# Kernel optimization log

Hardware: AMD Instinct MI355X
Metric: run time of the kernel (lower is better)

## Reference

```python
import jax, jax.numpy as jnp
import numpy as np
import math

HIDDEN = 2048
HEADS = 16
HEAD_DIM = HIDDEN // HEADS
MAX_SEQ = 4096
ROPE_BASE = 10000.0


def rope_cos_sin(seq_len):
    # (seq_len, head_dim//2) angle table
    inv_freq = 1.0 / (ROPE_BASE ** (jnp.arange(0, HEAD_DIM, 2, dtype=jnp.float32) / HEAD_DIM))
    t = jnp.arange(seq_len, dtype=jnp.float32)
    ang = jnp.einsum('s,f->sf', t, inv_freq)
    return jnp.cos(ang), jnp.sin(ang)


def apply_rope(x, cos, sin):
    # x: (b, s, h, d); interleaved complex pairs along last dim
    b, s, h, d = x.shape
    xr = x.reshape(b, s, h, d // 2, 2)
    x0, x1 = xr[..., 0], xr[..., 1]
    c = cos[:s][None, :, None, :]
    sn = sin[:s][None, :, None, :]
    o0 = x0 * c - x1 * sn
    o1 = x0 * sn + x1 * c
    return jnp.stack([o0, o1], axis=-1).reshape(b, s, h, d)


def setup_inputs() -> dict:
    key = jax.random.key(0)
    k1, k2, k3, k4, k5, k6 = jax.random.split(key, 6)
    B, SQ, SK = 2, 2048, 2048
    x = jax.random.normal(k1, (B, SQ, HIDDEN), dtype=jnp.float32)
    enc = jax.random.normal(k2, (B, SK, HIDDEN), dtype=jnp.float32)
    mask = jnp.ones((B, SK), dtype=jnp.int32)
    scale = 0.02
    Wq = jax.random.normal(k3, (HIDDEN, HIDDEN), dtype=jnp.float32) * scale
    Wk = jax.random.normal(k4, (HIDDEN, HIDDEN), dtype=jnp.float32) * scale
    Wv = jax.random.normal(k5, (HIDDEN, HIDDEN), dtype=jnp.float32) * scale
    Wo = jax.random.normal(k6, (HIDDEN, HIDDEN), dtype=jnp.float32) * scale
    return {"x": x, "encoder_output": enc, "encoder_attention_mask": mask,
            "Wq": Wq, "Wk": Wk, "Wv": Wv, "Wo": Wo}


def reference(x, encoder_output, encoder_attention_mask, Wq, Wk, Wv, Wo):
    B, SQ, _ = x.shape
    SK = encoder_output.shape[1]
    # nn.Linear(bias=False): y = x @ W^T
    q = (x @ Wq.T).reshape(B, SQ, HEADS, HEAD_DIM)
    k = (encoder_output @ Wk.T).reshape(B, SK, HEADS, HEAD_DIM)
    v = (encoder_output @ Wv.T).reshape(B, SK, HEADS, HEAD_DIM)
    cos, sin = rope_cos_sin(max(SQ, SK))
    q = apply_rope(q, cos, sin)
    k = apply_rope(k, cos, sin)
    scale = math.sqrt(HEAD_DIM)
    # (b, h, sq, sk) scores
    scores = jnp.einsum('bqhd,bkhd->bhqk', q, k) / scale
    mask = encoder_attention_mask[:, None, None, :]
    scores = jnp.where(mask == 0, -jnp.inf, scores)
    attn = jax.nn.softmax(scores, axis=-1)
    out = jnp.einsum('bhqk,bkhd->bqhd', attn, v).reshape(B, SQ, HIDDEN)
    return out @ Wo.T
```

## Files before the change

kernel.cpp:

```cpp
#include <hip/hip_runtime.h>
#include <stdint.h>


#define LOG2E 1.44269504088896340736f
#define INV2PI 0.15915494309189535f

typedef __attribute__((ext_vector_type(8))) short bf16x8;
typedef __attribute__((ext_vector_type(8))) uint16_t u16x8;
typedef __attribute__((ext_vector_type(4))) uint16_t u16x4;
typedef __attribute__((ext_vector_type(4))) float f32x4;

__device__ __forceinline__ uint16_t f2bf(float f) {
  union { float f; uint32_t i; } v; v.f = f;
  uint32_t x = v.i;
  return (uint16_t)((x + 0x7fffu + ((x >> 16) & 1u)) >> 16);
}
__device__ __forceinline__ uint32_t f_as_u(float f) { union { float f; uint32_t u; } v; v.f = f; return v.u; }
__device__ __forceinline__ float u_as_f(uint32_t u) { union { uint32_t u; float f; } v; v.u = u; return v.f; }
__device__ __forceinline__ void glds16(const void* g, void* l) {
  __builtin_amdgcn_global_load_lds((const __attribute__((address_space(1))) void*)g,
                                   (__attribute__((address_space(3))) void*)l, 16, 0, 0);
}

__global__ __launch_bounds__(256) void convert_f32_bf16(const float* __restrict__ in,
                                                        uint16_t* __restrict__ out) {
  const long i = ((long)blockIdx.x * 256 + threadIdx.x) * 8;
  const f32x4 a = *(const f32x4*)(in + i);
  const f32x4 b = *(const f32x4*)(in + i + 4);
  u16x8 o;
#pragma unroll
  for (int j = 0; j < 4; ++j) { o[j] = f2bf(a[j]); o[4 + j] = f2bf(b[j]); }
  *(u16x8*)(out + i) = o;
}

__global__ __launch_bounds__(256) void mask_bias(const int* __restrict__ m,
                                                 float* __restrict__ bias) {
  const int i = blockIdx.x * 256 + threadIdx.x;
  bias[i] = m[i] ? 0.0f : -__builtin_inff();
}

#define EPI_ROPE 0
#define EPI_KV   1
#define EPI_F32  2

__device__ __forceinline__ void epi_rope_store(uint16_t* C, const f32x4& a, int rowbase,
                                               int col, int N, float oscale) {
  const int f = (col >> 1) & 63;
  const float inv = __builtin_amdgcn_exp2f((float)f * (-13.287712379549449f / 64.0f));
  const float sgn = (col & 1) ? 1.0f : -1.0f;
#pragma unroll
  for (int r = 0; r < 4; ++r) {
    const float val = a[r];
    const float partner = __shfl_xor(val, 1);
    const int s = (rowbase + r) & 2047;
    const float rev = __builtin_amdgcn_fractf((float)s * inv * INV2PI);
    const float sn = __builtin_amdgcn_sinf(rev);
    const float cs = __builtin_amdgcn_cosf(rev);
    C[(long)(rowbase + r) * N + col] = f2bf((val * cs + sgn * partner * sn) * oscale);
  }
}

template <int MODE>
__global__ __launch_bounds__(256) void gemm_bt(const uint16_t* __restrict__ A,
                                               const uint16_t* __restrict__ W0,
                                               const uint16_t* __restrict__ W1,
                                               void* __restrict__ C0v,
                                               void* __restrict__ C1v,
                                               int M, int N, int K, float oscale) {
  __shared__ __align__(16) uint16_t As[2][128 * 32];
  __shared__ __align__(16) uint16_t Bs[2][128 * 32];
  const int tid = threadIdx.x;
  const int lane = tid & 63;
  const int w = tid >> 6;
  const int r16 = lane & 15, quad = lane >> 4;
  const int m0 = blockIdx.y * 128, n0 = blockIdx.x * 128;
  const int wm = (w >> 1) * 64, wn = (w & 1) * 64;
  f32x4 acc[4][4] = {};
  const int srow = 32 * w + (lane >> 2);
  const int scol = (lane & 3) * 8;
  const uint16_t* Wbase = (MODE == EPI_KV && n0 >= 2048) ? W1 + (long)(n0 - 2048) * K
                                                         : W0 + (long)n0 * K;
  const uint16_t* Ag = A + (long)(m0 + srow) * K + scol;
  const uint16_t* Wg = Wbase + (long)srow * K + scol;
  const int co = 2 * w * 512;

  glds16(Ag, &As[0][co]);
  glds16(Ag + (long)16 * K, &As[0][co + 512]);
  glds16(Wg, &Bs[0][co]);
  glds16(Wg + (long)16 * K, &Bs[0][co + 512]);

  auto body = [&](int k1, const uint16_t* Ac, const uint16_t* Bc,
                  uint16_t* An, uint16_t* Bn, bool pf) {
    __syncthreads();
    if (pf) {
      glds16(Ag + k1, An + co);
      glds16(Ag + k1 + (long)16 * K, An + co + 512);
      glds16(Wg + k1, Bn + co);
      glds16(Wg + k1 + (long)16 * K, Bn + co + 512);
    }
    bf16x8 af[4], bfr[4];
#pragma unroll
    for (int mt = 0; mt < 4; ++mt)
      af[mt] = *(const bf16x8*)(Ac + (wm + mt * 16 + r16) * 32 + quad * 8);
#pragma unroll
    for (int nt = 0; nt < 4; ++nt)
      bfr[nt] = *(const bf16x8*)(Bc + (wn + nt * 16 + r16) * 32 + quad * 8);
#pragma unroll
    for (int mt = 0; mt < 4; ++mt)
#pragma unroll
      for (int nt = 0; nt < 4; ++nt)
        acc[mt][nt] = __builtin_amdgcn_mfma_f32_16x16x32_bf16(af[mt], bfr[nt], acc[mt][nt], 0, 0, 0);
  };

  const int NK2 = K >> 6;
  for (int kk = 0; kk < NK2; ++kk) {
    body((2 * kk + 1) * 32, &As[0][0], &Bs[0][0], &As[1][0], &Bs[1][0], true);
    body((2 * kk + 2) * 32, &As[1][0], &Bs[1][0], &As[0][0], &Bs[0][0], kk < NK2 - 1);
  }

#pragma unroll
  for (int mt = 0; mt < 4; ++mt)
#pragma unroll
    for (int nt = 0; nt < 4; ++nt) {
      const int col = n0 + wn + nt * 16 + r16;
      const int rowbase = m0 + wm + mt * 16 + quad * 4;
      if constexpr (MODE == EPI_F32) {
        float* C = (float*)C0v;
#pragma unroll
        for (int r = 0; r < 4; ++r)
          C[(long)(rowbase + r) * N + col] = acc[mt][nt][r];
      } else if constexpr (MODE == EPI_ROPE) {
        epi_rope_store((uint16_t*)C0v, acc[mt][nt], rowbase, col, N, oscale);
      } else {
        if (n0 < 2048) {
          epi_rope_store((uint16_t*)C0v, acc[mt][nt], rowbase, col, 2048, 1.0f);
        } else {
          uint16_t* Vt = (uint16_t*)C1v;
          const int c = col - 2048;
          const int h = c >> 7, d = c & 127;
          const int b = rowbase >> 11, s = rowbase & 2047;
          u16x4 pk;
#pragma unroll
          for (int r = 0; r < 4; ++r) pk[r] = f2bf(acc[mt][nt][r]);
          *(u16x4*)(Vt + (long)((b * 16 + h) * 128 + d) * 2048 + s) = pk;
        }
      }
    }
}

__global__ __launch_bounds__(256) void attn_kernel(const uint16_t* __restrict__ Q,
                                                   const uint16_t* __restrict__ K,
                                                   const uint16_t* __restrict__ Vt,
                                                   const float* __restrict__ bias,
                                                   uint16_t* __restrict__ O) {
  __shared__ __align__(16) uint16_t Ks[2][32 * 128];
  __shared__ __align__(16) uint16_t Vts[2][128 * 32];
  __shared__ __align__(16) uint16_t Ps[4][32 * 40];
  const int tid = threadIdx.x;
  const int lane = tid & 63;
  const int w = tid >> 6;
  const int r16 = lane & 15, quad = lane >> 4;
  const int h = blockIdx.y, b = blockIdx.z;
  const int qbase = blockIdx.x * 128 + w * 32;

  bf16x8 qf[2][4];
#pragma unroll
  for (int t = 0; t < 2; ++t) {
    const uint16_t* qb = Q + ((long)(b * 2048 + qbase + t * 16 + r16)) * 2048 + h * 128 + quad * 8;
#pragma unroll
    for (int c = 0; c < 4; ++c) qf[t][c] = *(const bf16x8*)(qb + c * 32);
  }
  f32x4 oacc[2][8] = {};
  float li[2][4] = {};

  uint16_t* PsW = &Ps[w][0];
  const float* brow = bias + b * 2048;

  const int key0[2] = {8 * w + quad, 8 * w + 4 + quad};
  const uint16_t* kg[2];
  const uint16_t* vg[2];
#pragma unroll
  for (int i = 0; i < 2; ++i) {
    kg[i] = K + ((long)(b * 2048 + key0[i])) * 2048 + h * 128 + 8 * (r16 ^ ((4 * i + quad) & 7));
    const int dim = 32 * w + 16 * i + (lane >> 2);
    vg[i] = Vt + ((long)((b * 16 + h) * 128 + dim)) * 2048 + 8 * ((lane & 3) ^ ((lane >> 2) & 3));
  }

#pragma unroll
  for (int i = 0; i < 2; ++i) {
    glds16(kg[i], &Ks[0][(2 * w + i) * 512]);
    glds16(vg[i], &Vts[0][(2 * w + i) * 512]);
    kg[i] += 32 * 2048;
    vg[i] += 32;
  }
  float bn0 = brow[r16], bn1 = brow[16 + r16];

  auto body = [&](int k0, const uint16_t* Kc, const uint16_t* Vc,
                  uint16_t* Kn, uint16_t* Vn, bool pf) {
    __syncthreads();
    const float bc0 = bn0, bc1 = bn1;
    if (pf) {
#pragma unroll
      for (int i = 0; i < 2; ++i) {
        glds16(kg[i], Kn + (2 * w + i) * 512);
        glds16(vg[i], Vn + (2 * w + i) * 512);
        kg[i] += 32 * 2048;
        vg[i] += 32;
      }
      bn0 = brow[k0 + 32 + r16];
      bn1 = brow[k0 + 48 + r16];
    }
#pragma unroll
    for (int ct = 0; ct < 2; ++ct) {
      const int key = ct * 16 + r16;
      const int kb = key & 7;
      bf16x8 kf[4];
#pragma unroll
      for (int c = 0; c < 4; ++c)
        kf[c] = *(const bf16x8*)(Kc + key * 128 + ((4 * c + quad) ^ kb) * 8);
      const float bv = ct ? bc1 : bc0;
      const int pc = ct * 2 + (r16 >> 3);
#pragma unroll
      for (int t = 0; t < 2; ++t) {
        f32x4 s = {};
#pragma unroll
        for (int c = 0; c < 4; ++c)
          s = __builtin_amdgcn_mfma_f32_16x16x32_bf16(qf[t][c], kf[c], s, 0, 0, 0);
#pragma unroll
        for (int r = 0; r < 4; ++r) {
          const float p = __builtin_amdgcn_exp2f(s[r] + bv);
          const uint32_t pb = f_as_u(p) + 0x8000u;
          const int row = t * 16 + quad * 4 + r;
          PsW[row * 40 + ((pc ^ r) << 3) + (r16 & 7)] = (uint16_t)(pb >> 16);
          li[t][r] += u_as_f(pb & 0xffff0000u);
        }
      }
    }
    bf16x8 pa[2];
#pragma unroll
    for (int t = 0; t < 2; ++t)
      pa[t] = *(const bf16x8*)(PsW + (t * 16 + r16) * 40 + ((quad ^ (r16 & 3)) << 3));
#pragma unroll
    for (int nt = 0; nt < 8; ++nt) {
      const int dim = nt * 16 + r16;
      bf16x8 vf = *(const bf16x8*)(Vc + dim * 32 + ((quad ^ (dim & 3)) << 3));
#pragma unroll
      for (int t = 0; t < 2; ++t)
        oacc[t][nt] = __builtin_amdgcn_mfma_f32_16x16x32_bf16(pa[t], vf, oacc[t][nt], 0, 0, 0);
    }
  };

  for (int kt2 = 0; kt2 < 32; ++kt2) {
    body(64 * kt2,      &Ks[0][0], &Vts[0][0], &Ks[1][0], &Vts[1][0], true);
    body(64 * kt2 + 32, &Ks[1][0], &Vts[1][0], &Ks[0][0], &Vts[0][0], kt2 < 31);
  }

#pragma unroll
  for (int off = 1; off < 16; off <<= 1)
#pragma unroll
    for (int t = 0; t < 2; ++t)
#pragma unroll
      for (int r = 0; r < 4; ++r) li[t][r] += __shfl_xor(li[t][r], off);

#pragma unroll
  for (int t = 0; t < 2; ++t) {
    uint16_t* ob = O + ((long)(b * 2048 + qbase + t * 16)) * 2048 + h * 128;
    float inv_l[4];
#pragma unroll
    for (int r = 0; r < 4; ++r) inv_l[r] = 1.0f / li[t][r];
#pragma unroll
    for (int nt = 0; nt < 8; ++nt)
#pragma unroll
      for (int r = 0; r < 4; ++r)
        ob[(long)(quad * 4 + r) * 2048 + nt * 16 + r16] = f2bf(oacc[t][nt][r] * inv_l[r]);
  }
}

extern "C" void kernel_launch(void* const* d_in, const int* in_sizes, int n_in,
                              void* d_out, int out_size, void* d_ws, size_t ws_size,
                              hipStream_t stream) {
  const float* x   = (const float*)d_in[0];
  const float* enc = (const float*)d_in[1];
  const int*   msk = (const int*)d_in[2];
  const float* Wq  = (const float*)d_in[3];
  const float* Wk  = (const float*)d_in[4];
  const float* Wv  = (const float*)d_in[5];
  const float* Wo  = (const float*)d_in[6];
  float* out = (float*)d_out;

  const long NELT = 8L * 1024 * 1024;
  const long WELT = 4L * 1024 * 1024;
  uint16_t* Qb   = (uint16_t*)d_ws;
  uint16_t* Kb   = Qb + NELT;
  uint16_t* Vtb  = Kb + NELT;
  uint16_t* xb   = Vtb + NELT;
  uint16_t* encb = xb + NELT;
  uint16_t* Wb   = encb + NELT;
  uint16_t* Wvb  = xb;
  uint16_t* Ob   = xb;
  float*    biasb = (float*)encb;

  const float cs_exp = 0.088388347648318447f * LOG2E;

  const int CB_ACT = (int)(NELT / 2048);
  const int CB_W   = (int)(WELT / 2048);

  convert_f32_bf16<<<CB_ACT, 256, 0, stream>>>(x, xb);
  convert_f32_bf16<<<CB_W, 256, 0, stream>>>(Wq, Wb);
  gemm_bt<EPI_ROPE><<<dim3(16, 32), 256, 0, stream>>>(xb, Wb, nullptr, Qb, nullptr,
                                                      4096, 2048, 2048, cs_exp);

  convert_f32_bf16<<<CB_ACT, 256, 0, stream>>>(enc, encb);
  convert_f32_bf16<<<CB_W, 256, 0, stream>>>(Wk, Wb);
  convert_f32_bf16<<<CB_W, 256, 0, stream>>>(Wv, Wvb);
  gemm_bt<EPI_KV><<<dim3(32, 32), 256, 0, stream>>>(encb, Wb, Wvb, Kb, Vtb,
                                                    4096, 4096, 2048, 1.0f);

  mask_bias<<<16, 256, 0, stream>>>(msk, biasb);

  attn_kernel<<<dim3(16, 16, 2), 256, 0, stream>>>(Qb, Kb, Vtb, biasb, Ob);

  convert_f32_bf16<<<CB_W, 256, 0, stream>>>(Wo, Wb);
  gemm_bt<EPI_F32><<<dim3(16, 32), 256, 0, stream>>>(Ob, Wb, nullptr, out, nullptr,
                                                     4096, 2048, 2048, 1.0f);
}
```

Before: 484.5 us.

## Merge Q and KV projections into one GEMM launch and batch weight conversion

The Q projection and the fused K/V projection now run as a single 6144-wide GEMM. Each column block picks x or the encoder output as its A operand and routes its epilogue to Q (RoPE plus scale), K (RoPE) or transposed V. All four weight matrices are converted to bf16 by one kernel into a contiguous buffer. The bf16 activation copies are staged in the output buffer as scratch. This cuts kernel launches and gives the projection step one larger grid with less wave-quantization tail, at the cost of more workspace for all four bf16 weights.

```diff
diff --git a/kernel.cpp b/kernel.cpp
--- a/kernel.cpp
+++ b/kernel.cpp
@@ -33,21 +33,37 @@
   *(u16x8*)(out + i) = o;
 }
 
+__global__ __launch_bounds__(256) void convert_w4(const float* __restrict__ Wq,
+                                                  const float* __restrict__ Wk,
+                                                  const float* __restrict__ Wv,
+                                                  const float* __restrict__ Wo,
+                                                  uint16_t* __restrict__ W4) {
+  const int blk = blockIdx.x;
+  const int sec = blk >> 11;
+  const long off = ((long)(blk & 2047) * 256 + threadIdx.x) * 8;
+  const float* src = (sec == 0) ? Wq : (sec == 1) ? Wk : (sec == 2) ? Wv : Wo;
+  const f32x4 a = *(const f32x4*)(src + off);
+  const f32x4 b = *(const f32x4*)(src + off + 4);
+  u16x8 o;
+#pragma unroll
+  for (int j = 0; j < 4; ++j) { o[j] = f2bf(a[j]); o[4 + j] = f2bf(b[j]); }
+  *(u16x8*)(W4 + (long)sec * 4194304 + off) = o;
+}
+
 __global__ __launch_bounds__(256) void mask_bias(const int* __restrict__ m,
                                                  float* __restrict__ bias) {
   const int i = blockIdx.x * 256 + threadIdx.x;
   bias[i] = m[i] ? 0.0f : -__builtin_inff();
 }
 
-#define EPI_ROPE 0
-#define EPI_KV   1
-#define EPI_F32  2
+#define EPI_QKV 0
+#define EPI_F32 1
 
 __device__ __forceinline__ void epi_rope_store(uint16_t* C, const f32x4& a, int rowbase,
-                                               int col, int N, float oscale) {
-  const int f = (col >> 1) & 63;
+                                               int c, float oscale) {
+  const int f = (c >> 1) & 63;
   const float inv = __builtin_amdgcn_exp2f((float)f * (-13.287712379549449f / 64.0f));
-  const float sgn = (col & 1) ? 1.0f : -1.0f;
+  const float sgn = (c & 1) ? 1.0f : -1.0f;
 #pragma unroll
   for (int r = 0; r < 4; ++r) {
     const float val = a[r];
@@ -56,16 +72,17 @@
     const float rev = __builtin_amdgcn_fractf((float)s * inv * INV2PI);
     const float sn = __builtin_amdgcn_sinf(rev);
     const float cs = __builtin_amdgcn_cosf(rev);
-    C[(long)(rowbase + r) * N + col] = f2bf((val * cs + sgn * partner * sn) * oscale);
+    C[(long)(rowbase + r) * 2048 + c] = f2bf((val * cs + sgn * partner * sn) * oscale);
   }
 }
 
 template <int MODE>
-__global__ __launch_bounds__(256) void gemm_bt(const uint16_t* __restrict__ A,
-                                               const uint16_t* __restrict__ W0,
-                                               const uint16_t* __restrict__ W1,
+__global__ __launch_bounds__(256) void gemm_bt(const uint16_t* __restrict__ A0,
+                                               const uint16_t* __restrict__ A1,
+                                               const uint16_t* __restrict__ W,
                                                void* __restrict__ C0v,
                                                void* __restrict__ C1v,
+                                               void* __restrict__ C2v,
                                                int M, int N, int K, float oscale) {
   __shared__ __align__(16) uint16_t As[2][128 * 32];
   __shared__ __align__(16) uint16_t Bs[2][128 * 32];
@@ -78,10 +95,9 @@
   f32x4 acc[4][4] = {};
   const int srow = 32 * w + (lane >> 2);
   const int scol = (lane & 3) * 8;
-  const uint16_t* Wbase = (MODE == EPI_KV && n0 >= 2048) ? W1 + (long)(n0 - 2048) * K
-                                                         : W0 + (long)n0 * K;
+  const uint16_t* A = (MODE == EPI_QKV && n0 >= 2048) ? A1 : A0;
   const uint16_t* Ag = A + (long)(m0 + srow) * K + scol;
-  const uint16_t* Wg = Wbase + (long)srow * K + scol;
+  const uint16_t* Wg = W + (long)(n0 + srow) * K + scol;
   const int co = 2 * w * 512;
 
   glds16(Ag, &As[0][co]);
@@ -129,14 +145,14 @@
 #pragma unroll
         for (int r = 0; r < 4; ++r)
           C[(long)(rowbase + r) * N + col] = acc[mt][nt][r];
-      } else if constexpr (MODE == EPI_ROPE) {
-        epi_rope_store((uint16_t*)C0v, acc[mt][nt], rowbase, col, N, oscale);
       } else {
         if (n0 < 2048) {
-          epi_rope_store((uint16_t*)C0v, acc[mt][nt], rowbase, col, 2048, 1.0f);
+          epi_rope_store((uint16_t*)C0v, acc[mt][nt], rowbase, col, oscale);
+        } else if (n0 < 4096) {
+          epi_rope_store((uint16_t*)C1v, acc[mt][nt], rowbase, col - 2048, 1.0f);
         } else {
-          uint16_t* Vt = (uint16_t*)C1v;
-          const int c = col - 2048;
+          uint16_t* Vt = (uint16_t*)C2v;
+          const int c = col - 4096;
           const int h = c >> 7, d = c & 127;
           const int b = rowbase >> 11, s = rowbase & 2047;
           u16x4 pk;
@@ -290,37 +306,28 @@
 
   const long NELT = 8L * 1024 * 1024;
   const long WELT = 4L * 1024 * 1024;
-  uint16_t* Qb   = (uint16_t*)d_ws;
-  uint16_t* Kb   = Qb + NELT;
-  uint16_t* Vtb  = Kb + NELT;
-  uint16_t* xb   = Vtb + NELT;
+  uint16_t* Qb  = (uint16_t*)d_ws;
+  uint16_t* Kb  = Qb + NELT;
+  uint16_t* Vtb = Kb + NELT;
+  uint16_t* W4  = Vtb + NELT;
+  float* biasb  = (float*)(W4 + 4 * WELT);
+  uint16_t* xb   = (uint16_t*)d_out;
   uint16_t* encb = xb + NELT;
-  uint16_t* Wb   = encb + NELT;
-  uint16_t* Wvb  = xb;
-  uint16_t* Ob   = xb;
-  float*    biasb = (float*)encb;
+  uint16_t* Ob   = W4;
 
   const float cs_exp = 0.088388347648318447f * LOG2E;
 
-  const int CB_ACT = (int)(NELT / 2048);
-  const int CB_W   = (int)(WELT / 2048);
-
-  convert_f32_bf16<<<CB_ACT, 256, 0, stream>>>(x, xb);
-  convert_f32_bf16<<<CB_W, 256, 0, stream>>>(Wq, Wb);
-  gemm_bt<EPI_ROPE><<<dim3(16, 32), 256, 0, stream>>>(xb, Wb, nullptr, Qb, nullptr,
-                                                      4096, 2048, 2048, cs_exp);
-
-  convert_f32_bf16<<<CB_ACT, 256, 0, stream>>>(enc, encb);
-  convert_f32_bf16<<<CB_W, 256, 0, stream>>>(Wk, Wb);
-  convert_f32_bf16<<<CB_W, 256, 0, stream>>>(Wv, Wvb);
-  gemm_bt<EPI_KV><<<dim3(32, 32), 256, 0, stream>>>(encb, Wb, Wvb, Kb, Vtb,
-                                                    4096, 4096, 2048, 1.0f);
-
+  convert_f32_bf16<<<(int)(NELT / 2048), 256, 0, stream>>>(x, xb);
+  convert_f32_bf16<<<(int)(NELT / 2048), 256, 0, stream>>>(enc, encb);
+  convert_w4<<<8192, 256, 0, stream>>>(Wq, Wk, Wv, Wo, W4);
   mask_bias<<<16, 256, 0, stream>>>(msk, biasb);
 
+  gemm_bt<EPI_QKV><<<dim3(48, 32), 256, 0, stream>>>(xb, encb, W4, Qb, Kb, Vtb,
+                                                     4096, 6144, 2048, cs_exp);
+
   attn_kernel<<<dim3(16, 16, 2), 256, 0, stream>>>(Qb, Kb, Vtb, biasb, Ob);
 
-  convert_f32_bf16<<<CB_W, 256, 0, stream>>>(Wo, Wb);
-  gemm_bt<EPI_F32><<<dim3(16, 32), 256, 0, stream>>>(Ob, Wb, nullptr, out, nullptr,
+  gemm_bt<EPI_F32><<<dim3(16, 32), 256, 0, stream>>>(Ob, nullptr, W4 + 3 * WELT,
+                                                     out, nullptr, nullptr,
                                                      4096, 2048, 2048, 1.0f);
 }
```

After: 478.9 us. About the same (-1.2%).
